# Kernel tuning notes

Hardware: AMD Instinct MI355X
Metric: run time of the kernel (lower is better)

Reference implementation:

```python
import jax, jax.numpy as jnp
import numpy as np


def _euclidean_cdist(x, q):
    # torch.cdist with p=2: pairwise L2 distances, shape [B, Q]
    x2 = jnp.sum(x * x, axis=-1, keepdims=True)          # [B, 1]
    q2 = jnp.sum(q * q, axis=-1)[None, :]                # [1, Q]
    d2 = x2 + q2 - 2.0 * (x @ q.T)                        # [B, Q]
    return jnp.sqrt(jnp.maximum(d2, 0.0))


def setup_inputs() -> dict:
    key = jax.random.key(0)
    k1, k2 = jax.random.split(key)
    x = jax.random.normal(k1, (1024, 256), dtype=jnp.float32)
    queue = jax.random.normal(k2, (32768, 256), dtype=jnp.float32)
    return {"x": x, "queue": queue}


def reference(x, queue):
    # Queue update: concat then keep the newest max_size rows (queue assumed full)
    max_size = queue.shape[0]
    q = jnp.concatenate([queue, x], axis=0)[-max_size:]   # [Q, F]
    # Distance matrix + top-2 nearest (topk of negated distances)
    d = _euclidean_cdist(x, q)                            # [B, Q]
    _, idx = jax.lax.top_k(-d, 2)                         # [B, 2]
    # Second-nearest neighbor (first is the point itself, dist 0)
    return q[idx[:, 1]]                                   # [B, F]
```

## Files before the change

### kernel.cpp

```cpp
#include <hip/hip_runtime.h>
#include <stdint.h>

#define B_ROWS 1024
#define FEAT   256
#define QSZ    32768
#define SHIFT  1024
#define QX     (QSZ - B_ROWS)
#define NQB    256
#define MARGIN 8.0f

typedef float v4f __attribute__((ext_vector_type(4)));
typedef short v8s __attribute__((ext_vector_type(8)));

__device__ __forceinline__ uint32_t key_flip(uint32_t u) {
    return u ^ ((uint32_t)((int32_t)u >> 31) | 0x80000000u);
}
__device__ __forceinline__ float key_m(uint32_t k) {
    uint32_t u = k & 0xFFFF8000u;
    u = (u & 0x80000000u) ? (u ^ 0x80000000u) : ~u;
    return __uint_as_float(u);
}
__device__ __forceinline__ void k2_insert(uint32_t& k1, uint32_t& k2, uint32_t key) {
    uint32_t hi = max(k1, key); k1 = min(k1, key); k2 = min(k2, hi);
}
__device__ __forceinline__ uint2 k2_merge(uint2 a, uint2 b) {
    uint32_t hi = max(a.x, b.x);
    uint2 r; r.x = min(a.x, b.x); r.y = min(min(a.y, b.y), hi);
    return r;
}

struct Top2 { float m1; int j1; float m2; int j2; };
__device__ __forceinline__ bool better(float ma, int ja, float mb, int jb) {
    return (ma < mb) || (ma == mb && ja < jb);
}
__device__ __forceinline__ void t2_insert(Top2& t, float m, int j) {
    if (better(m, j, t.m1, t.j1)) { t.m2 = t.m1; t.j2 = t.j1; t.m1 = m; t.j1 = j; }
    else if (better(m, j, t.m2, t.j2)) { t.m2 = m; t.j2 = j; }
}

__device__ __forceinline__ const float* q_row_ptr(int j, const float* x, const float* queue) {
    return (j < QX) ? (queue + (size_t)(j + SHIFT) * FEAT) : (x + (size_t)(j - QX) * FEAT);
}

__device__ __forceinline__ unsigned short f2bf(float f) {
    uint32_t u = __float_as_uint(f);
    uint32_t r = u + 0x7FFFu + ((u >> 16) & 1u);
    return (unsigned short)(r >> 16);
}

__device__ __forceinline__ void lds_load16(const void* g, void* l) {
    __builtin_amdgcn_global_load_lds(
        (const __attribute__((address_space(1))) uint32_t*)g,
        (__attribute__((address_space(3))) uint32_t*)l, 16, 0, 0);
}

__global__ __launch_bounds__(256) void convert_kernel(const float* __restrict__ x,
                                                      const float* __restrict__ queue,
                                                      unsigned short* __restrict__ q_bf,
                                                      float* __restrict__ q2) {
    int wave = threadIdx.x >> 6, lane = threadIdx.x & 63;
    int j = blockIdx.x * 4 + wave;
    const float4* row = (const float4*)q_row_ptr(j, x, queue);
    float4 v = row[lane];
    float s = v.x * v.x + v.y * v.y + v.z * v.z + v.w * v.w;
#pragma unroll
    for (int off = 32; off; off >>= 1) s += __shfl_xor(s, off, 64);
    if (lane == 0) q2[j] = s;
    ushort4 h;
    h.x = f2bf(v.x); h.y = f2bf(v.y); h.z = f2bf(v.z); h.w = f2bf(v.w);
    ((ushort4*)q_bf)[(size_t)j * 64 + lane] = h;
}

__global__ __launch_bounds__(256, 2) void nn_mfma(const unsigned short* __restrict__ q_bf,
                                                  const float* __restrict__ q2,
                                                  uint2* __restrict__ partials) {
    __shared__ unsigned short As[128 * 256];

    const int t    = threadIdx.x;
    const int w    = t >> 6, lane = t & 63;
    const int wm   = w >> 1, wn = w & 1;
    const int quad = lane >> 4, l16 = lane & 15;
    const int c3   = l16 & 7;

    const int id = blockIdx.x;
    const int s_ = id >> 3;
    const int gy = (id & 7) * 32 + (s_ & 31);
    const int gx = s_ >> 5;

    const unsigned short* x_bf  = q_bf + (size_t)QX * FEAT;
    const unsigned short* aBase = q_bf + (size_t)gy * 128 * FEAT;
    const unsigned short* bBase = x_bf + (size_t)gx * 128 * FEAT;

    v8s fb[4][8];
#pragma unroll
    for (int tn = 0; tn < 4; ++tn) {
        const unsigned short* brow = bBase + (size_t)(wn * 64 + tn * 16 + l16) * FEAT + quad * 8;
#pragma unroll
        for (int ks = 0; ks < 8; ++ks)
            fb[tn][ks] = *(const v8s*)(brow + ks * 32);
    }

#pragma unroll
    for (int i = 0; i < 16; ++i) {
        int rowp = w * 32 + i * 2;
        int row  = rowp + (lane >> 5);
        int g    = (lane & 31) ^ (row & 7);
        lds_load16(aBase + (size_t)row * FEAT + g * 8, &As[rowp * 256]);
    }

    v4f acc[4][4];
#pragma unroll
    for (int a = 0; a < 4; ++a)
#pragma unroll
        for (int b = 0; b < 4; ++b) acc[a][b] = (v4f)0.0f;

    __syncthreads();

#pragma unroll
    for (int ks = 0; ks < 8; ++ks) {
        const int gofs = (((ks * 4 + quad) ^ c3) << 4);
        v8s fa[4];
#pragma unroll
        for (int tm = 0; tm < 4; ++tm)
            fa[tm] = *(const v8s*)((const char*)As + (wm * 64 + tm * 16 + l16) * 512 + gofs);
#pragma unroll
        for (int tm = 0; tm < 4; ++tm)
#pragma unroll
            for (int tn = 0; tn < 4; ++tn)
                acc[tm][tn] = __builtin_amdgcn_mfma_f32_16x16x32_bf16(fa[tm], fb[tn][ks], acc[tm][tn], 0, 0, 0);
    }

    const int jbase = gy * 128 + wm * 64 + quad * 4;
    float q2r[4][4];
#pragma unroll
    for (int tm = 0; tm < 4; ++tm) {
        v4f qq = *(const v4f*)(q2 + jbase + tm * 16);
#pragma unroll
        for (int r = 0; r < 4; ++r) q2r[tm][r] = qq[r];
    }

    uint2 best[4];
#pragma unroll
    for (int tn = 0; tn < 4; ++tn) {
        uint32_t k1 = 0xFFFFFFFFu, k2 = 0xFFFFFFFFu;
#pragma unroll
        for (int tm = 0; tm < 4; ++tm)
#pragma unroll
            for (int r = 0; r < 4; ++r) {
                float m = fmaf(-2.0f, acc[tm][tn][r], q2r[tm][r]);
                uint32_t u = key_flip(__float_as_uint(m));
                uint32_t key = (u & 0xFFFF8000u) | (uint32_t)(jbase + tm * 16 + r);
                k2_insert(k1, k2, key);
            }
#pragma unroll
        for (int mask = 16; mask <= 32; mask <<= 1) {
            uint32_t o1 = __shfl_xor(k1, mask, 64);
            uint32_t o2 = __shfl_xor(k2, mask, 64);
            uint32_t hi = max(k1, o1);
            k1 = min(k1, o1);
            k2 = min(min(k2, o2), hi);
        }
        best[tn] = make_uint2(k1, k2);
    }
    __syncthreads();
    uint2* scr = (uint2*)As;
    if (quad == 0) {
#pragma unroll
        for (int tn = 0; tn < 4; ++tn)
            scr[(wn * 64 + tn * 16 + l16) * 2 + wm] = best[tn];
    }
    __syncthreads();
    if (t < 128) {
        uint2 r = k2_merge(scr[t * 2], scr[t * 2 + 1]);
        partials[(size_t)(gx * 128 + t) * NQB + gy] = r;
    }
}

__global__ __launch_bounds__(64) void nn_finalize(const float* __restrict__ x,
                                                  const float* __restrict__ queue,
                                                  const float* __restrict__ q2,
                                                  const uint2* __restrict__ partials,
                                                  float* __restrict__ out) {
    __shared__ int list[64];
    __shared__ int s_cnt;

    const int i = blockIdx.x, lane = threadIdx.x;
    if (lane == 0) s_cnt = 0;

    const uint2* p = partials + (size_t)i * NQB;
    uint2 mine[4];
#pragma unroll
    for (int u = 0; u < 4; ++u) mine[u] = p[lane + 64 * u];
    uint2 a = k2_merge(k2_merge(mine[0], mine[1]), k2_merge(mine[2], mine[3]));
#pragma unroll
    for (int mask = 1; mask <= 32; mask <<= 1) {
        uint2 o;
        o.x = __shfl_xor(a.x, mask, 64);
        o.y = __shfl_xor(a.y, mask, 64);
        a = k2_merge(a, o);
    }
    float cutf = key_m(a.y) + MARGIN;
    uint32_t kcut = key_flip(__float_as_uint(cutf)) | 0x7FFFu;

#pragma unroll
    for (int u = 0; u < 4; ++u) {
        if (mine[u].x <= kcut) list[atomicAdd(&s_cnt, 1) & 63] = (int)(mine[u].x & 0x7FFFu);
        if (mine[u].y <= kcut) list[atomicAdd(&s_cnt, 1) & 63] = (int)(mine[u].y & 0x7FFFu);
    }
    __syncthreads();
    int n = min(s_cnt, 64);

    float4 xv = ((const float4*)(x + (size_t)i * FEAT))[lane];
    Top2 bst;
    bst.m1 = __builtin_inff(); bst.j1 = 0x7FFFFFFF;
    bst.m2 = __builtin_inff(); bst.j2 = 0x7FFFFFFF;
    for (int c = 0; c < n; ++c) {
        int j = list[c];
        float4 qv = ((const float4*)q_row_ptr(j, x, queue))[lane];
        float s = qv.x * xv.x + qv.y * xv.y + qv.z * xv.z + qv.w * xv.w;
#pragma unroll
        for (int off = 32; off; off >>= 1) s += __shfl_xor(s, off, 64);
        float m = q2[j] - 2.0f * s;
        t2_insert(bst, m, j);
    }
    int j2 = bst.j2;
    float4 o = ((const float4*)q_row_ptr(j2, x, queue))[lane];
    ((float4*)(out + (size_t)i * FEAT))[lane] = o;
}

extern "C" void kernel_launch(void* const* d_in, const int* in_sizes, int n_in,
                              void* d_out, int out_size, void* d_ws, size_t ws_size,
                              hipStream_t stream) {
    const float* x     = (const float*)d_in[0];
    const float* queue = (const float*)d_in[1];

    unsigned short* q_bf     = (unsigned short*)d_ws;
    float*          q2       = (float*)((char*)d_ws + (16u << 20));
    uint2*          partials = (uint2*)((char*)d_ws + (17u << 20));

    convert_kernel<<<QSZ / 4, 256, 0, stream>>>(x, queue, q_bf, q2);
    nn_mfma<<<2048, 256, 0, stream>>>(q_bf, q2, partials);
    nn_finalize<<<B_ROWS, 64, 0, stream>>>(x, queue, q2, partials, (float*)d_out);
}
```

Measured before the change: 134.1 us.

## Drop LDS staging in MFMA kernel, use smaller 128x64 tiles with register double-buffering

```diff
diff --git a/kernel.cpp b/kernel.cpp
--- a/kernel.cpp
+++ b/kernel.cpp
@@ -46,12 +46,6 @@
     uint32_t u = __float_as_uint(f);
     uint32_t r = u + 0x7FFFu + ((u >> 16) & 1u);
     return (unsigned short)(r >> 16);
-}
-
-__device__ __forceinline__ void lds_load16(const void* g, void* l) {
-    __builtin_amdgcn_global_load_lds(
-        (const __attribute__((address_space(1))) uint32_t*)g,
-        (__attribute__((address_space(3))) uint32_t*)l, 16, 0, 0);
 }
 
 __global__ __launch_bounds__(256) void convert_kernel(const float* __restrict__ x,
@@ -71,69 +65,65 @@
     ((ushort4*)q_bf)[(size_t)j * 64 + lane] = h;
 }
 
-__global__ __launch_bounds__(256, 2) void nn_mfma(const unsigned short* __restrict__ q_bf,
+__global__ __launch_bounds__(256, 4) void nn_mfma(const unsigned short* __restrict__ q_bf,
                                                   const float* __restrict__ q2,
                                                   uint2* __restrict__ partials) {
-    __shared__ unsigned short As[128 * 256];
+    __shared__ uint2 scr[64][4];
 
     const int t    = threadIdx.x;
     const int w    = t >> 6, lane = t & 63;
-    const int wm   = w >> 1, wn = w & 1;
     const int quad = lane >> 4, l16 = lane & 15;
-    const int c3   = l16 & 7;
 
     const int id = blockIdx.x;
-    const int s_ = id >> 3;
-    const int gy = (id & 7) * 32 + (s_ & 31);
-    const int gx = s_ >> 5;
-
-    const unsigned short* x_bf  = q_bf + (size_t)QX * FEAT;
-    const unsigned short* aBase = q_bf + (size_t)gy * 128 * FEAT;
-    const unsigned short* bBase = x_bf + (size_t)gx * 128 * FEAT;
-
-    v8s fb[4][8];
-#pragma unroll
-    for (int tn = 0; tn < 4; ++tn) {
-        const unsigned short* brow = bBase + (size_t)(wn * 64 + tn * 16 + l16) * FEAT + quad * 8;
-#pragma unroll
-        for (int ks = 0; ks < 8; ++ks)
-            fb[tn][ks] = *(const v8s*)(brow + ks * 32);
-    }
-
-#pragma unroll
-    for (int i = 0; i < 16; ++i) {
-        int rowp = w * 32 + i * 2;
-        int row  = rowp + (lane >> 5);
-        int g    = (lane & 31) ^ (row & 7);
-        lds_load16(aBase + (size_t)row * FEAT + g * 8, &As[rowp * 256]);
-    }
-
-    v4f acc[4][4];
-#pragma unroll
-    for (int a = 0; a < 4; ++a)
+    const int u_ = id >> 3;
+    const int gy = (id & 7) * 32 + (u_ & 31);
+    const int gx = u_ >> 5;
+
+    const unsigned short* x_bf = q_bf + (size_t)QX * FEAT;
+
+    const unsigned short* aptr0 = q_bf + (size_t)(gy * 128 + w * 32 + l16) * FEAT + quad * 8;
+    const unsigned short* aptr1 = aptr0 + 16 * FEAT;
+    const unsigned short* bptr[4];
+#pragma unroll
+    for (int tn = 0; tn < 4; ++tn)
+        bptr[tn] = x_bf + (size_t)(gx * 64 + tn * 16 + l16) * FEAT + quad * 8;
+
+    v4f acc[2][4];
+#pragma unroll
+    for (int a = 0; a < 2; ++a)
 #pragma unroll
         for (int b = 0; b < 4; ++b) acc[a][b] = (v4f)0.0f;
 
-    __syncthreads();
+    v8s fa0[2], fb0[4], fa1[2], fb1[4];
+    fa0[0] = *(const v8s*)(aptr0);
+    fa0[1] = *(const v8s*)(aptr1);
+#pragma unroll
+    for (int tn = 0; tn < 4; ++tn) fb0[tn] = *(const v8s*)(bptr[tn]);
 
 #pragma unroll
     for (int ks = 0; ks < 8; ++ks) {
-        const int gofs = (((ks * 4 + quad) ^ c3) << 4);
-        v8s fa[4];
-#pragma unroll
-        for (int tm = 0; tm < 4; ++tm)
-            fa[tm] = *(const v8s*)((const char*)As + (wm * 64 + tm * 16 + l16) * 512 + gofs);
-#pragma unroll
-        for (int tm = 0; tm < 4; ++tm)
+        v8s (&fa)[2] = (ks & 1) ? fa1 : fa0;
+        v8s (&fb)[4] = (ks & 1) ? fb1 : fb0;
+        v8s (&na)[2] = (ks & 1) ? fa0 : fa1;
+        v8s (&nb)[4] = (ks & 1) ? fb0 : fb1;
+        if (ks < 7) {
+            na[0] = *(const v8s*)(aptr0 + (ks + 1) * 32);
+            na[1] = *(const v8s*)(aptr1 + (ks + 1) * 32);
 #pragma unroll
             for (int tn = 0; tn < 4; ++tn)
-                acc[tm][tn] = __builtin_amdgcn_mfma_f32_16x16x32_bf16(fa[tm], fb[tn][ks], acc[tm][tn], 0, 0, 0);
-    }
-
-    const int jbase = gy * 128 + wm * 64 + quad * 4;
-    float q2r[4][4];
-#pragma unroll
-    for (int tm = 0; tm < 4; ++tm) {
+                nb[tn] = *(const v8s*)(bptr[tn] + (ks + 1) * 32);
+        }
+#pragma unroll
+        for (int tm = 0; tm < 2; ++tm)
+#pragma unroll
+            for (int tn = 0; tn < 4; ++tn)
+                acc[tm][tn] = __builtin_amdgcn_mfma_f32_16x16x32_bf16(fa[tm], fb[tn], acc[tm][tn], 0, 0, 0);
+    }
+
+    const int jbase = gy * 128 + w * 32 + quad * 4;
+    float q2r[2][4];
+#pragma unroll
+    for (int tm = 0; tm < 2; ++tm) {
         v4f qq = *(const v4f*)(q2 + jbase + tm * 16);
 #pragma unroll
         for (int r = 0; r < 4; ++r) q2r[tm][r] = qq[r];
@@ -144,7 +134,7 @@
     for (int tn = 0; tn < 4; ++tn) {
         uint32_t k1 = 0xFFFFFFFFu, k2 = 0xFFFFFFFFu;
 #pragma unroll
-        for (int tm = 0; tm < 4; ++tm)
+        for (int tm = 0; tm < 2; ++tm)
 #pragma unroll
             for (int r = 0; r < 4; ++r) {
                 float m = fmaf(-2.0f, acc[tm][tn][r], q2r[tm][r]);
@@ -162,17 +152,15 @@
         }
         best[tn] = make_uint2(k1, k2);
     }
+    if (quad == 0) {
+#pragma unroll
+        for (int tn = 0; tn < 4; ++tn) scr[tn * 16 + l16][w] = best[tn];
+    }
     __syncthreads();
-    uint2* scr = (uint2*)As;
-    if (quad == 0) {
-#pragma unroll
-        for (int tn = 0; tn < 4; ++tn)
-            scr[(wn * 64 + tn * 16 + l16) * 2 + wm] = best[tn];
-    }
-    __syncthreads();
-    if (t < 128) {
-        uint2 r = k2_merge(scr[t * 2], scr[t * 2 + 1]);
-        partials[(size_t)(gx * 128 + t) * NQB + gy] = r;
+    if (t < 64) {
+        uint2 r = k2_merge(k2_merge(scr[t][0], scr[t][1]),
+                           k2_merge(scr[t][2], scr[t][3]));
+        partials[(size_t)(gx * 64 + t) * NQB + gy] = r;
     }
 }
 
@@ -239,6 +227,6 @@
     uint2*          partials = (uint2*)((char*)d_ws + (17u << 20));
 
     convert_kernel<<<QSZ / 4, 256, 0, stream>>>(x, queue, q_bf, q2);
-    nn_mfma<<<2048, 256, 0, stream>>>(q_bf, q2, partials);
+    nn_mfma<<<4096, 256, 0, stream>>>(q_bf, q2, partials);
     nn_finalize<<<B_ROWS, 64, 0, stream>>>(x, queue, q2, partials, (float*)d_out);
 }
```

Result: slower. 179.2 us (+33.6%).
